# Optimization experiments

Measured on AMD Instinct MI355X. Metric: run time of the kernel, lower is better.

## Reference

```python
import jax, jax.numpy as jnp
import numpy as np

B, P, R_BAR, WIDTH, ADD_WIDTH, KERNEL_WIDTH = 4096, 1024, 64, 1024, 64, 16
NEG_SLOPE = 0.1

def leaky(x):
    return jnp.where(x > 0, x, NEG_SLOPE * x)

def setup_inputs() -> dict:
    key = jax.random.key(0)
    ks = jax.random.split(key, 16)
    s = lambda fan_in: 1.0 / np.sqrt(fan_in)
    return {
        "x": jax.random.normal(ks[0], (B, P), jnp.float32),
        # PCA layer 1: Linear(p -> r_bar), stored [in, out]
        "W_pca": jax.random.normal(ks[1], (P, R_BAR), jnp.float32) * s(P),
        "b_pca": jnp.zeros((R_BAR,), jnp.float32),
        # relu_stack: Linear(r_bar -> width), Linear(width -> width)
        "W1": jax.random.normal(ks[2], (R_BAR, WIDTH), jnp.float32) * s(R_BAR),
        "b1": jnp.zeros((WIDTH,), jnp.float32),
        "W2": jax.random.normal(ks[3], (WIDTH, WIDTH), jnp.float32) * s(WIDTH),
        "b2": jnp.zeros((WIDTH,), jnp.float32),
        # AdditiveLayer 1: r_bar tiny Linears (kernel_width -> add_width), batched [r, in, out]
        "add1_W": jax.random.normal(ks[4], (R_BAR, KERNEL_WIDTH, ADD_WIDTH), jnp.float32) * s(KERNEL_WIDTH),
        "add1_b": jnp.zeros((R_BAR, ADD_WIDTH), jnp.float32),
        "add1_bias": jnp.zeros((1,), jnp.float32),
        # AdditiveLayer 2: r_bar Linears (add_width -> add_width)
        "add2_W": jax.random.normal(ks[5], (R_BAR, ADD_WIDTH, ADD_WIDTH), jnp.float32) * s(ADD_WIDTH),
        "add2_b": jnp.zeros((R_BAR, ADD_WIDTH), jnp.float32),
        "add2_bias": jnp.zeros((1,), jnp.float32),
        # PCA layer 2: Linear(r_bar*add_width -> r_bar)
        "W_pca2": jax.random.normal(ks[6], (R_BAR * ADD_WIDTH, R_BAR), jnp.float32) * s(R_BAR * ADD_WIDTH),
        "b_pca2": jnp.zeros((R_BAR,), jnp.float32),
        # last layer: Linear(r_bar -> 1)
        "W_last": jax.random.normal(ks[7], (R_BAR, 1), jnp.float32) * s(R_BAR),
        "b_last": jnp.zeros((1,), jnp.float32),
    }

def reference(x, W_pca, b_pca, W1, b1, W2, b2,
              add1_W, add1_b, add1_bias,
              add2_W, add2_b, add2_bias,
              W_pca2, b_pca2, W_last, b_last):
    # PcaLayer 1 (cov/trace bookkeeping does not affect the output)
    t = x @ W_pca + b_pca                                   # [B, r_bar]
    # relu_stack (nn_depth = 2)
    h = leaky(t @ W1 + b1)                                   # [B, width]
    h = leaky(h @ W2 + b2)                                   # [B, width]
    # AdditiveLayer 1: modulo-gather kernel_width cols per slot, batched tiny GEMMs
    idx1 = jnp.arange(R_BAR * KERNEL_WIDTH) % h.shape[1]
    g1 = h[:, idx1].reshape(-1, R_BAR, KERNEL_WIDTH)         # [B, r, kw]
    a = jnp.einsum('brk,rko->bro', g1, add1_W) + add1_b      # [B, r, add_w]
    a = leaky(a.reshape(a.shape[0], -1) + add1_bias)         # [B, r*add_w]
    # AdditiveLayer 2: slices are contiguous (mod is identity) -> plain reshape
    g2 = a.reshape(-1, R_BAR, ADD_WIDTH)
    a2 = jnp.einsum('bri,rio->bro', g2, add2_W) + add2_b
    a2 = leaky(a2.reshape(a2.shape[0], -1) + add2_bias)      # [B, r*add_w]
    # PcaLayer 2 + last layer
    t2 = a2 @ W_pca2 + b_pca2                                # [B, r_bar]
    out = (t2 @ W_last + b_last).reshape(-1, 1)              # [B, 1]
    return out
```

## Files before the change

### kernel.cpp

```cpp
#include <hip/hip_runtime.h>

#define NEG_SLOPE 0.1f

__device__ __forceinline__ float leaky(float v) { return v > 0.0f ? v : NEG_SLOPE * v; }

typedef _Float16 h4_t __attribute__((ext_vector_type(4)));
typedef _Float16 h8_t __attribute__((ext_vector_type(8)));
typedef float f32x4 __attribute__((ext_vector_type(4)));

__device__ __forceinline__ unsigned lds_off(const void* p) {
    return (unsigned)(unsigned long long)p;
}

__device__ __forceinline__ void lgkm0() {
    asm volatile("s_waitcnt lgkmcnt(0)" ::: "memory");
    __builtin_amdgcn_sched_barrier(0);
}

__device__ __forceinline__ h4_t tr16(unsigned addr) {
    h4_t d;
    asm volatile("ds_read_b64_tr_b16 %0, %1" : "=v"(d) : "v"(addr) : "memory");
    return d;
}

__global__ __launch_bounds__(256) void prep_weights(const float* __restrict__ W2,
                                                    const float* __restrict__ W1,
                                                    const float* __restrict__ a1W,
                                                    const float* __restrict__ a2W,
                                                    const float* __restrict__ Wp2,
                                                    _Float16* __restrict__ W2T,
                                                    _Float16* __restrict__ W1T,
                                                    _Float16* __restrict__ wpack)
{
    __shared__ float tile[32][33];
    const int b   = blockIdx.x;
    const int tid = threadIdx.x;

    if (b < 1024) {
        const int n0 = (b & 31) * 32, k0 = (b >> 5) * 32;
        const int r = tid >> 3, c4 = (tid & 7) * 4;
        float4 v = *reinterpret_cast<const float4*>(&W2[(size_t)(k0 + r) * 1024 + n0 + c4]);
        tile[r][c4 + 0] = v.x; tile[r][c4 + 1] = v.y;
        tile[r][c4 + 2] = v.z; tile[r][c4 + 3] = v.w;
        __syncthreads();
        h4_t o;
        o[0] = (_Float16)tile[c4 + 0][r]; o[1] = (_Float16)tile[c4 + 1][r];
        o[2] = (_Float16)tile[c4 + 2][r]; o[3] = (_Float16)tile[c4 + 3][r];
        *reinterpret_cast<h4_t*>(&W2T[(size_t)(n0 + r) * 1024 + k0 + c4]) = o;
    } else if (b < 1088) {
        const int b2 = b - 1024;
        const int n0 = (b2 & 31) * 32, k0 = (b2 >> 5) * 32;
        const int r = tid >> 3, c4 = (tid & 7) * 4;
        float4 v = *reinterpret_cast<const float4*>(&W1[(size_t)(k0 + r) * 1024 + n0 + c4]);
        tile[r][c4 + 0] = v.x; tile[r][c4 + 1] = v.y;
        tile[r][c4 + 2] = v.z; tile[r][c4 + 3] = v.w;
        __syncthreads();
        h4_t o;
        o[0] = (_Float16)tile[c4 + 0][r]; o[1] = (_Float16)tile[c4 + 1][r];
        o[2] = (_Float16)tile[c4 + 2][r]; o[3] = (_Float16)tile[c4 + 3][r];
        *reinterpret_cast<h4_t*>(&W1T[(size_t)(n0 + r) * 64 + k0 + c4]) = o;
    } else {
        const int idx = (b - 1088) * 256 + tid;
        if (idx < 589824) {
            const int r = idx / 9216, qq = idx % 9216;
            float v;
            if (qq < 1024) {
                int nt = qq >> 8, rem = qq & 255, l = rem >> 2, j = rem & 3;
                int n = nt * 16 + (l & 15), k = (l >> 4) * 4 + j;
                v = a1W[(size_t)r * 1024 + k * 64 + n];
            } else if (qq < 5120) {
                int p = qq - 1024, kt = p >> 11, u = p & 2047, nt = u >> 9, s = u & 511,
                    l = s >> 3, j = s & 7;
                int n = nt * 16 + (l & 15), k = kt * 32 + (l >> 4) * 8 + j;
                v = a2W[(size_t)r * 4096 + k * 64 + n];
            } else {
                int p = qq - 5120, kt = p >> 11, u = p & 2047, nt = u >> 9, s = u & 511,
                    l = s >> 3, j = s & 7;
                int n = nt * 16 + (l & 15), k = kt * 32 + (l >> 4) * 8 + j;
                v = Wp2[((size_t)r * 64 + k) * 64 + n];
            }
            wpack[idx] = (_Float16)v;
        }
    }
}

__global__ __launch_bounds__(256) void gemm_n64_splitk(const float* __restrict__ A,
                                                       const float* __restrict__ B,
                                                       float* __restrict__ P)
{
    __shared__ alignas(16) float As[32][33];
    __shared__ alignas(16) float Bs[32][64];
    const int tid   = threadIdx.x;
    const int row0  = blockIdx.x * 32;
    const int kbase = blockIdx.y * 128;
    const int r0    = (tid >> 4) * 2;
    const int c0    = (tid & 15) * 4;
    const int am    = tid >> 3;
    const int ak    = (tid & 7) * 4;
    float acc[2][4] = {};

#pragma unroll
    for (int kc = 0; kc < 128; kc += 32) {
        const int k0 = kbase + kc;
        float4 va = *reinterpret_cast<const float4*>(&A[(size_t)(row0 + am) * 1024 + k0 + ak]);
        As[ak + 0][am] = va.x; As[ak + 1][am] = va.y;
        As[ak + 2][am] = va.z; As[ak + 3][am] = va.w;
#pragma unroll
        for (int p = 0; p < 2; ++p) {
            int idx = tid + p * 256;
            int kk  = idx >> 4;
            int nq  = (idx & 15) * 4;
            *reinterpret_cast<float4*>(&Bs[kk][nq]) =
                *reinterpret_cast<const float4*>(&B[(size_t)(k0 + kk) * 64 + nq]);
        }
        __syncthreads();
#pragma unroll
        for (int k = 0; k < 32; ++k) {
            float a0 = As[k][r0], a1 = As[k][r0 + 1];
            float4 bv = *reinterpret_cast<const float4*>(&Bs[k][c0]);
            acc[0][0] = fmaf(a0, bv.x, acc[0][0]); acc[0][1] = fmaf(a0, bv.y, acc[0][1]);
            acc[0][2] = fmaf(a0, bv.z, acc[0][2]); acc[0][3] = fmaf(a0, bv.w, acc[0][3]);
            acc[1][0] = fmaf(a1, bv.x, acc[1][0]); acc[1][1] = fmaf(a1, bv.y, acc[1][1]);
            acc[1][2] = fmaf(a1, bv.z, acc[1][2]); acc[1][3] = fmaf(a1, bv.w, acc[1][3]);
        }
        __syncthreads();
    }
#pragma unroll
    for (int i = 0; i < 2; ++i) {
        float4 o; o.x = acc[i][0]; o.y = acc[i][1]; o.z = acc[i][2]; o.w = acc[i][3];
        *reinterpret_cast<float4*>(
            &P[((size_t)blockIdx.y * 4096 + row0 + r0 + i) * 64 + c0]) = o;
    }
}

__global__ __launch_bounds__(256) void combine_t16(const float* __restrict__ P,
                                                   const float* __restrict__ bias,
                                                   _Float16* __restrict__ t16)
{
    const int idx = blockIdx.x * 256 + threadIdx.x;
    float s = bias[idx & 63];
#pragma unroll
    for (int c = 0; c < 8; ++c)
        s += P[(size_t)c * 262144 + idx];
    t16[idx] = (_Float16)s;
}

__global__ __launch_bounds__(256) void gemm_k64_mfma(const _Float16* __restrict__ A,
                                                     const _Float16* __restrict__ BT,
                                                     const float* __restrict__ bias,
                                                     _Float16* __restrict__ C)
{
    __shared__ alignas(16) _Float16 As[128 * 64];
    __shared__ alignas(16) _Float16 Bs[128 * 64];
    const int tid = threadIdx.x;
    const int l   = tid & 63;
    const int w   = tid >> 6;
    const int wm  = w >> 1;
    const int wn  = w & 1;
    const int bm0 = blockIdx.y * 128;
    const int bn0 = blockIdx.x * 128;
    const int fr  = l & 15;
    const int fg  = l >> 4;
    const int srow  = l >> 3;
    const int sslot = l & 7;

#pragma unroll
    for (int i = 0; i < 4; ++i) {
        const int r0   = w * 32 + i * 8;
        const int rowA = r0 + srow;
        const int slot = sslot ^ (rowA & 7);
        __builtin_amdgcn_global_load_lds(
            (const __attribute__((address_space(1))) void*)&A[(size_t)(bm0 + rowA) * 64 + slot * 8],
            (__attribute__((address_space(3))) void*)&As[r0 * 64], 16, 0, 0);
        __builtin_amdgcn_global_load_lds(
            (const __attribute__((address_space(1))) void*)&BT[(size_t)(bn0 + rowA) * 64 + slot * 8],
            (__attribute__((address_space(3))) void*)&Bs[r0 * 64], 16, 0, 0);
    }
    __syncthreads();

    f32x4 acc[4][4] = {};
#pragma unroll
    for (int ks = 0; ks < 2; ++ks) {
        h8_t af[4], bf[4];
#pragma unroll
        for (int mt = 0; mt < 4; ++mt) {
            int row = wm * 64 + mt * 16 + fr;
            int sg  = ks * 4 + fg;
            af[mt] = *reinterpret_cast<const h8_t*>(&As[row * 64 + ((sg ^ (row & 7)) << 3)]);
        }
#pragma unroll
        for (int nt = 0; nt < 4; ++nt) {
            int row = wn * 64 + nt * 16 + fr;
            int sg  = ks * 4 + fg;
            bf[nt] = *reinterpret_cast<const h8_t*>(&Bs[row * 64 + ((sg ^ (row & 7)) << 3)]);
        }
#pragma unroll
        for (int mt = 0; mt < 4; ++mt)
#pragma unroll
            for (int nt = 0; nt < 4; ++nt)
                acc[mt][nt] = __builtin_amdgcn_mfma_f32_16x16x32_f16(af[mt], bf[nt],
                                                                     acc[mt][nt], 0, 0, 0);
    }

#pragma unroll
    for (int nt = 0; nt < 4; ++nt) {
        const int col = bn0 + wn * 64 + nt * 16 + fr;
        const float bv = bias[col];
#pragma unroll
        for (int mt = 0; mt < 4; ++mt)
#pragma unroll
            for (int rg = 0; rg < 4; ++rg) {
                const int row = bm0 + wm * 64 + mt * 16 + fg * 4 + rg;
                float v = acc[mt][nt][rg] + bv;
                C[(size_t)row * 1024 + col] = (_Float16)fmaxf(v, NEG_SLOPE * v);
            }
    }
}

__global__ __launch_bounds__(256) void gemm_mfma_f16(const _Float16* __restrict__ A,
                                                     const _Float16* __restrict__ BT,
                                                     const float* __restrict__ bias,
                                                     _Float16* __restrict__ h2t)
{
    __shared__ alignas(16) _Float16 As[128 * 32];
    __shared__ alignas(16) _Float16 Bs[128 * 32];
    const int tid = threadIdx.x;
    const int l   = tid & 63;
    const int w   = tid >> 6;
    const int wm  = w >> 1;
    const int wn  = w & 1;
    const int bm0 = blockIdx.y * 128;
    const int bn0 = blockIdx.x * 128;
    const int fr  = l & 15;
    const int fg  = l >> 4;
    const int srow  = l >> 2;
    const int sslot = l & 3;

    f32x4 acc[4][4] = {};

    for (int k0 = 0; k0 < 1024; k0 += 32) {
#pragma unroll
        for (int i = 0; i < 2; ++i) {
            const int r0   = (w * 2 + i) * 16;
            const int rowA = r0 + srow;
            const int slot = sslot ^ (rowA & 3);
            __builtin_amdgcn_global_load_lds(
                (const __attribute__((address_space(1))) void*)&A[(size_t)(bm0 + rowA) * 1024 + k0 + slot * 8],
                (__attribute__((address_space(3))) void*)&As[r0 * 32], 16, 0, 0);
            __builtin_amdgcn_global_load_lds(
                (const __attribute__((address_space(1))) void*)&BT[(size_t)(bn0 + rowA) * 1024 + k0 + slot * 8],
                (__attribute__((address_space(3))) void*)&Bs[r0 * 32], 16, 0, 0);
        }
        __syncthreads();

        h8_t af[4], bf[4];
#pragma unroll
        for (int mt = 0; mt < 4; ++mt) {
            int row = wm * 64 + mt * 16 + fr;
            af[mt] = *reinterpret_cast<const h8_t*>(&As[row * 32 + ((fg ^ (row & 3)) << 3)]);
        }
#pragma unroll
        for (int nt = 0; nt < 4; ++nt) {
            int row = wn * 64 + nt * 16 + fr;
            bf[nt] = *reinterpret_cast<const h8_t*>(&Bs[row * 32 + ((fg ^ (row & 3)) << 3)]);
        }
#pragma unroll
        for (int mt = 0; mt < 4; ++mt)
#pragma unroll
            for (int nt = 0; nt < 4; ++nt)
                acc[mt][nt] = __builtin_amdgcn_mfma_f32_16x16x32_f16(af[mt], bf[nt],
                                                                     acc[mt][nt], 0, 0, 0);
        __syncthreads();
    }

    const int rblk0 = (bm0 >> 4) + wm * 4;
    const int cblk0 = (bn0 >> 4) + wn * 4;
#pragma unroll
    for (int nt = 0; nt < 4; ++nt) {
        const int col = bn0 + wn * 64 + nt * 16 + fr;
        const float bv = bias[col];
#pragma unroll
        for (int mt = 0; mt < 4; ++mt) {
            h4_t pk;
#pragma unroll
            for (int r = 0; r < 4; ++r) {
                float v = acc[mt][nt][r] + bv;
                pk[r] = (_Float16)fmaxf(v, NEG_SLOPE * v);
            }
            *reinterpret_cast<h4_t*>(
                &h2t[(((size_t)(cblk0 + nt) * 256 + rblk0 + mt) * 16 + fr) * 16 + fg * 4]) = pk;
        }
    }
}

#define RCH 4

__global__ __launch_bounds__(256) void fused_tail4(const _Float16* __restrict__ h2t,
                                                   const _Float16* __restrict__ wpack,
                                                   const float* __restrict__ a1b,
                                                   const float* __restrict__ a1bias,
                                                   const float* __restrict__ a2b,
                                                   const float* __restrict__ a2bias,
                                                   float* __restrict__ partials)
{
    __shared__ alignas(16) _Float16 stage[2][10240];
    __shared__ alignas(16) _Float16 act[4][1024];

    const int tid = threadIdx.x;
    const int l = tid & 63, w = tid >> 6;
    const int c = l & 15, q = l >> 4;
    const int row0  = blockIdx.x * 64;
    const int rbase = blockIdx.y * RCH;
    const float b1s = a1bias[0], b2s = a2bias[0];

    const unsigned trl   = l * 8;
    const unsigned abase = lds_off(&act[w][0]);

    float b1v[RCH][4], b2v[RCH][4];
#pragma unroll
    for (int rl = 0; rl < RCH; ++rl)
#pragma unroll
        for (int nt = 0; nt < 4; ++nt) {
            b1v[rl][nt] = a1b[(rbase + rl) * 64 + nt * 16 + c] + b1s;
            b2v[rl][nt] = a2b[(rbase + rl) * 64 + nt * 16 + c] + b2s;
        }

    auto STAGE = [&](int rl, int b) {
        const int r = rbase + rl;
        const _Float16* hsrc = h2t + ((size_t)r * 256 + blockIdx.x * 4) * 256;
        const _Float16* wsrc = wpack + (size_t)r * 9216;
#pragma unroll
        for (int i = 0; i < 5; ++i) {
            const int ch = w * 5 + i;
            const _Float16* src = (ch < 2) ? (hsrc + ch * 512) : (wsrc + (ch - 2) * 512);
            __builtin_amdgcn_global_load_lds(
                (const __attribute__((address_space(1))) void*)(src + l * 8),
                (__attribute__((address_space(3))) void*)&stage[b][ch * 512], 16, 0, 0);
        }
    };

    STAGE(0, 0);
    __syncthreads();

    f32x4 accT[4] = {};
    int cur = 0;

#pragma unroll
    for (int rl = 0; rl < RCH; ++rl) {
        if (rl + 1 < RCH) STAGE(rl + 1, cur ^ 1);

        const _Float16* sp = &stage[cur][0];
        const unsigned sbytes = lds_off(sp);

        h4_t ha = tr16(sbytes + w * 512 + trl);
        lgkm0();
        f32x4 pa[4];
#pragma unroll
        for (int nt = 0; nt < 4; ++nt) {
            h4_t bf = *reinterpret_cast<const h4_t*>(&sp[1024 + nt * 256 + l * 4]);
            pa[nt] = __builtin_amdgcn_mfma_f32_16x16x16f16(ha, bf, (f32x4){0.f,0.f,0.f,0.f}, 0, 0, 0);
        }
#pragma unroll
        for (int nt = 0; nt < 4; ++nt) {
            h4_t pk;
#pragma unroll
            for (int rg = 0; rg < 4; ++rg) {
                float v = pa[nt][rg] + b1v[rl][nt];
                pk[rg] = (_Float16)fmaxf(v, NEG_SLOPE * v);
            }
            const int kk = nt * 16 + c;
            const int hh = (kk >> 2) & 1;
            const int kp = (kk & 3) | ((kk >> 3) << 2);
            *reinterpret_cast<h4_t*>(&act[w][hh * 512 + kp * 16 + q * 4]) = pk;
        }
        lgkm0();

        h8_t afB[2];
#pragma unroll
        for (int kt = 0; kt < 2; ++kt) {
            h4_t lo = tr16(abase + kt * 512 + trl);
            h4_t hi = tr16(abase + 1024 + kt * 512 + trl);
            afB[kt] = __builtin_shufflevector(lo, hi, 0, 1, 2, 3, 4, 5, 6, 7);
        }
        lgkm0();
        f32x4 pb[4] = {};
#pragma unroll
        for (int kt = 0; kt < 2; ++kt)
#pragma unroll
            for (int nt = 0; nt < 4; ++nt) {
                h8_t bf = *reinterpret_cast<const h8_t*>(&sp[2048 + kt * 2048 + nt * 512 + l * 8]);
                pb[nt] = __builtin_amdgcn_mfma_f32_16x16x32_f16(afB[kt], bf, pb[nt], 0, 0, 0);
            }
#pragma unroll
        for (int nt = 0; nt < 4; ++nt) {
            h4_t pk;
#pragma unroll
            for (int rg = 0; rg < 4; ++rg) {
                float v = pb[nt][rg] + b2v[rl][nt];
                pk[rg] = (_Float16)fmaxf(v, NEG_SLOPE * v);
            }
            const int kk = nt * 16 + c;
            const int hh = (kk >> 2) & 1;
            const int kp = (kk & 3) | ((kk >> 3) << 2);
            *reinterpret_cast<h4_t*>(&act[w][hh * 512 + kp * 16 + q * 4]) = pk;
        }
        lgkm0();

        h8_t afC[2];
#pragma unroll
        for (int kt = 0; kt < 2; ++kt) {
            h4_t lo = tr16(abase + kt * 512 + trl);
            h4_t hi = tr16(abase + 1024 + kt * 512 + trl);
            afC[kt] = __builtin_shufflevector(lo, hi, 0, 1, 2, 3, 4, 5, 6, 7);
        }
        lgkm0();
#pragma unroll
        for (int kt = 0; kt < 2; ++kt)
#pragma unroll
            for (int nt = 0; nt < 4; ++nt) {
                h8_t bf = *reinterpret_cast<const h8_t*>(&sp[6144 + kt * 2048 + nt * 512 + l * 8]);
                accT[nt] = __builtin_amdgcn_mfma_f32_16x16x32_f16(afC[kt], bf, accT[nt], 0, 0, 0);
            }

        __syncthreads();
        cur ^= 1;
    }

#pragma unroll
    for (int nt = 0; nt < 4; ++nt)
#pragma unroll
        for (int rg = 0; rg < 4; ++rg)
            partials[((size_t)blockIdx.y * 4096 + row0 + w * 16 + q * 4 + rg) * 64 + nt * 16 + c] =
                accT[nt][rg];
}

__global__ __launch_bounds__(256) void reduce_out(const float* __restrict__ partials,
                                                  const float* __restrict__ bp2,
                                                  const float* __restrict__ Wl,
                                                  const float* __restrict__ bl,
                                                  float* __restrict__ out)
{
    const int tid = threadIdx.x;
    const int row = blockIdx.x * 4 + (tid >> 6);
    const int col = tid & 63;
    float s = bp2[col];
#pragma unroll
    for (int c = 0; c < 16; ++c)
        s += partials[(size_t)c * 262144 + (size_t)row * 64 + col];
    s *= Wl[col];
    s += __shfl_xor(s, 1);
    s += __shfl_xor(s, 2);
    s += __shfl_xor(s, 4);
    s += __shfl_xor(s, 8);
    s += __shfl_xor(s, 16);
    s += __shfl_xor(s, 32);
    if (col == 0) out[row] = s + bl[0];
}

extern "C" void kernel_launch(void* const* d_in, const int* in_sizes, int n_in,
                              void* d_out, int out_size, void* d_ws, size_t ws_size,
                              hipStream_t stream)
{
    const float* x      = (const float*)d_in[0];
    const float* Wpca   = (const float*)d_in[1];
    const float* bpca   = (const float*)d_in[2];
    const float* W1     = (const float*)d_in[3];
    const float* b1     = (const float*)d_in[4];
    const float* W2     = (const float*)d_in[5];
    const float* b2     = (const float*)d_in[6];
    const float* a1W    = (const float*)d_in[7];
    const float* a1b    = (const float*)d_in[8];
    const float* a1bias = (const float*)d_in[9];
    const float* a2W    = (const float*)d_in[10];
    const float* a2b    = (const float*)d_in[11];
    const float* a2bias = (const float*)d_in[12];
    const float* Wp2    = (const float*)d_in[13];
    const float* bp2    = (const float*)d_in[14];
    const float* Wl     = (const float*)d_in[15];
    const float* bl     = (const float*)d_in[16];
    float* out = (float*)d_out;

    char* wsb = (char*)d_ws;
    _Float16* t16      = (_Float16*)(wsb);
    _Float16* h1h      = (_Float16*)(wsb + (1ull  << 20));
    _Float16* h2t      = (_Float16*)(wsb + (9ull  << 20));
    _Float16* W2T      = (_Float16*)(wsb + (17ull << 20));
    _Float16* wpack    = (_Float16*)(wsb + (19ull << 20));
    _Float16* W1T      = (_Float16*)(wsb + (21ull << 20));
    float*    partials = (float*)   (wsb + (22ull << 20));
    float*    tpart    = (float*)   (wsb + (9ull  << 20));

    prep_weights<<<dim3(3392), 256, 0, stream>>>(W2, W1, a1W, a2W, Wp2, W2T, W1T, wpack);
    gemm_n64_splitk<<<dim3(128, 8), 256, 0, stream>>>(x, Wpca, tpart);
    combine_t16<<<dim3(1024), 256, 0, stream>>>(tpart, bpca, t16);
    gemm_k64_mfma<<<dim3(8, 32), 256, 0, stream>>>(t16, W1T, b1, h1h);
    gemm_mfma_f16<<<dim3(8, 32), 256, 0, stream>>>(h1h, W2T, b2, h2t);
    fused_tail4<<<dim3(64, 16), 256, 0, stream>>>(h2t, wpack, a1b, a1bias,
                                                  a2b, a2bias, partials);
    reduce_out<<<dim3(1024), 256, 0, stream>>>(partials, bp2, Wl, bl, out);
}
```

Baseline: 73.58 us.

## Retile W2 GEMM to 64x128 with BK=64 and double rows per tail block

The 1024x1024 GEMM now uses 64x128 output tiles with a 64-deep K step and an 8-way XOR swizzle. This doubles the grid to 512 blocks, which fills the CUs better and halves the number of K iterations and barriers. The fused additive tail kernel now handles 128 batch rows per block instead of 64, so each staged weight tile is reused across two row groups. That halves the weight traffic into LDS, at the cost of more registers and LDS per block and half as many tail blocks.

New measurement: 65.10 us. 1.13x faster.

```diff
diff --git a/kernel.cpp b/kernel.cpp
--- a/kernel.cpp
+++ b/kernel.cpp
@@ -217,70 +217,81 @@
     }
 }
 
-__global__ __launch_bounds__(256) void gemm_mfma_f16(const _Float16* __restrict__ A,
-                                                     const _Float16* __restrict__ BT,
-                                                     const float* __restrict__ bias,
-                                                     _Float16* __restrict__ h2t)
-{
-    __shared__ alignas(16) _Float16 As[128 * 32];
-    __shared__ alignas(16) _Float16 Bs[128 * 32];
+__global__ __launch_bounds__(256) void gemm_mfma_f16_v2(const _Float16* __restrict__ A,
+                                                        const _Float16* __restrict__ BT,
+                                                        const float* __restrict__ bias,
+                                                        _Float16* __restrict__ h2t)
+{
+    __shared__ alignas(16) _Float16 As[64 * 64];
+    __shared__ alignas(16) _Float16 Bs[128 * 64];
     const int tid = threadIdx.x;
     const int l   = tid & 63;
     const int w   = tid >> 6;
     const int wm  = w >> 1;
     const int wn  = w & 1;
-    const int bm0 = blockIdx.y * 128;
+    const int bm0 = blockIdx.y * 64;
     const int bn0 = blockIdx.x * 128;
     const int fr  = l & 15;
     const int fg  = l >> 4;
-    const int srow  = l >> 2;
-    const int sslot = l & 3;
-
-    f32x4 acc[4][4] = {};
-
-    for (int k0 = 0; k0 < 1024; k0 += 32) {
+    const int srow  = l >> 3;
+    const int sslot = l & 7;
+
+    f32x4 acc[2][4] = {};
+
+    for (int k0 = 0; k0 < 1024; k0 += 64) {
 #pragma unroll
         for (int i = 0; i < 2; ++i) {
-            const int r0   = (w * 2 + i) * 16;
+            const int r0   = w * 16 + i * 8;
             const int rowA = r0 + srow;
-            const int slot = sslot ^ (rowA & 3);
+            const int slot = sslot ^ (rowA & 7);
             __builtin_amdgcn_global_load_lds(
                 (const __attribute__((address_space(1))) void*)&A[(size_t)(bm0 + rowA) * 1024 + k0 + slot * 8],
-                (__attribute__((address_space(3))) void*)&As[r0 * 32], 16, 0, 0);
+                (__attribute__((address_space(3))) void*)&As[r0 * 64], 16, 0, 0);
+        }
+#pragma unroll
+        for (int i = 0; i < 4; ++i) {
+            const int r0   = w * 32 + i * 8;
+            const int rowB = r0 + srow;
+            const int slot = sslot ^ (rowB & 7);
             __builtin_amdgcn_global_load_lds(
-                (const __attribute__((address_space(1))) void*)&BT[(size_t)(bn0 + rowA) * 1024 + k0 + slot * 8],
-                (__attribute__((address_space(3))) void*)&Bs[r0 * 32], 16, 0, 0);
-        }
-        __syncthreads();
-
-        h8_t af[4], bf[4];
-#pragma unroll
-        for (int mt = 0; mt < 4; ++mt) {
-            int row = wm * 64 + mt * 16 + fr;
-            af[mt] = *reinterpret_cast<const h8_t*>(&As[row * 32 + ((fg ^ (row & 3)) << 3)]);
-        }
-#pragma unroll
-        for (int nt = 0; nt < 4; ++nt) {
-            int row = wn * 64 + nt * 16 + fr;
-            bf[nt] = *reinterpret_cast<const h8_t*>(&Bs[row * 32 + ((fg ^ (row & 3)) << 3)]);
-        }
-#pragma unroll
-        for (int mt = 0; mt < 4; ++mt)
-#pragma unroll
-            for (int nt = 0; nt < 4; ++nt)
-                acc[mt][nt] = __builtin_amdgcn_mfma_f32_16x16x32_f16(af[mt], bf[nt],
-                                                                     acc[mt][nt], 0, 0, 0);
-        __syncthreads();
-    }
-
-    const int rblk0 = (bm0 >> 4) + wm * 4;
+                (const __attribute__((address_space(1))) void*)&BT[(size_t)(bn0 + rowB) * 1024 + k0 + slot * 8],
+                (__attribute__((address_space(3))) void*)&Bs[r0 * 64], 16, 0, 0);
+        }
+        __syncthreads();
+
+#pragma unroll
+        for (int ks = 0; ks < 2; ++ks) {
+            h8_t af[2], bf[4];
+#pragma unroll
+            for (int mt = 0; mt < 2; ++mt) {
+                int row = wm * 32 + mt * 16 + fr;
+                int sg  = ks * 4 + fg;
+                af[mt] = *reinterpret_cast<const h8_t*>(&As[row * 64 + ((sg ^ (row & 7)) << 3)]);
+            }
+#pragma unroll
+            for (int nt = 0; nt < 4; ++nt) {
+                int row = wn * 64 + nt * 16 + fr;
+                int sg  = ks * 4 + fg;
+                bf[nt] = *reinterpret_cast<const h8_t*>(&Bs[row * 64 + ((sg ^ (row & 7)) << 3)]);
+            }
+#pragma unroll
+            for (int mt = 0; mt < 2; ++mt)
+#pragma unroll
+                for (int nt = 0; nt < 4; ++nt)
+                    acc[mt][nt] = __builtin_amdgcn_mfma_f32_16x16x32_f16(af[mt], bf[nt],
+                                                                         acc[mt][nt], 0, 0, 0);
+        }
+        __syncthreads();
+    }
+
+    const int rblk0 = (bm0 >> 4) + wm * 2;
     const int cblk0 = (bn0 >> 4) + wn * 4;
 #pragma unroll
     for (int nt = 0; nt < 4; ++nt) {
         const int col = bn0 + wn * 64 + nt * 16 + fr;
         const float bv = bias[col];
 #pragma unroll
-        for (int mt = 0; mt < 4; ++mt) {
+        for (int mt = 0; mt < 2; ++mt) {
             h4_t pk;
 #pragma unroll
             for (int r = 0; r < 4; ++r) {
@@ -295,7 +306,7 @@
 
 #define RCH 4
 
-__global__ __launch_bounds__(256) void fused_tail4(const _Float16* __restrict__ h2t,
+__global__ __launch_bounds__(256) void fused_tail5(const _Float16* __restrict__ h2t,
                                                    const _Float16* __restrict__ wpack,
                                                    const float* __restrict__ a1b,
                                                    const float* __restrict__ a1bias,
@@ -303,13 +314,13 @@
                                                    const float* __restrict__ a2bias,
                                                    float* __restrict__ partials)
 {
-    __shared__ alignas(16) _Float16 stage[2][10240];
-    __shared__ alignas(16) _Float16 act[4][1024];
+    __shared__ alignas(16) _Float16 stage[2][11264];
+    __shared__ alignas(16) _Float16 act[4][2048];
 
     const int tid = threadIdx.x;
     const int l = tid & 63, w = tid >> 6;
     const int c = l & 15, q = l >> 4;
-    const int row0  = blockIdx.x * 64;
+    const int row0  = blockIdx.x * 128;
     const int rbase = blockIdx.y * RCH;
     const float b1s = a1bias[0], b2s = a2bias[0];
 
@@ -327,22 +338,24 @@
 
     auto STAGE = [&](int rl, int b) {
         const int r = rbase + rl;
-        const _Float16* hsrc = h2t + ((size_t)r * 256 + blockIdx.x * 4) * 256;
+        const _Float16* hsrc = h2t + ((size_t)r * 256 + blockIdx.x * 8) * 256;
         const _Float16* wsrc = wpack + (size_t)r * 9216;
 #pragma unroll
-        for (int i = 0; i < 5; ++i) {
-            const int ch = w * 5 + i;
-            const _Float16* src = (ch < 2) ? (hsrc + ch * 512) : (wsrc + (ch - 2) * 512);
-            __builtin_amdgcn_global_load_lds(
-                (const __attribute__((address_space(1))) void*)(src + l * 8),
-                (__attribute__((address_space(3))) void*)&stage[b][ch * 512], 16, 0, 0);
+        for (int i = 0; i < 6; ++i) {
+            const int ch = i * 4 + w;
+            if (ch < 22) {
+                const _Float16* src = (ch < 4) ? (hsrc + ch * 512) : (wsrc + (ch - 4) * 512);
+                __builtin_amdgcn_global_load_lds(
+                    (const __attribute__((address_space(1))) void*)(src + l * 8),
+                    (__attribute__((address_space(3))) void*)&stage[b][ch * 512], 16, 0, 0);
+            }
         }
     };
 
     STAGE(0, 0);
     __syncthreads();
 
-    f32x4 accT[4] = {};
+    f32x4 accT[2][4] = {};
     int cur = 0;
 
 #pragma unroll
@@ -352,74 +365,86 @@
         const _Float16* sp = &stage[cur][0];
         const unsigned sbytes = lds_off(sp);
 
-        h4_t ha = tr16(sbytes + w * 512 + trl);
+        h4_t ha0 = tr16(sbytes + (unsigned)(w) * 512 + trl);
+        h4_t ha1 = tr16(sbytes + (unsigned)(w + 4) * 512 + trl);
         lgkm0();
-        f32x4 pa[4];
+        f32x4 pa[2][4];
 #pragma unroll
         for (int nt = 0; nt < 4; ++nt) {
-            h4_t bf = *reinterpret_cast<const h4_t*>(&sp[1024 + nt * 256 + l * 4]);
-            pa[nt] = __builtin_amdgcn_mfma_f32_16x16x16f16(ha, bf, (f32x4){0.f,0.f,0.f,0.f}, 0, 0, 0);
-        }
-#pragma unroll
-        for (int nt = 0; nt < 4; ++nt) {
-            h4_t pk;
-#pragma unroll
-            for (int rg = 0; rg < 4; ++rg) {
-                float v = pa[nt][rg] + b1v[rl][nt];
-                pk[rg] = (_Float16)fmaxf(v, NEG_SLOPE * v);
-            }
-            const int kk = nt * 16 + c;
-            const int hh = (kk >> 2) & 1;
-            const int kp = (kk & 3) | ((kk >> 3) << 2);
-            *reinterpret_cast<h4_t*>(&act[w][hh * 512 + kp * 16 + q * 4]) = pk;
-        }
+            h4_t bf = *reinterpret_cast<const h4_t*>(&sp[2048 + nt * 256 + l * 4]);
+            pa[0][nt] = __builtin_amdgcn_mfma_f32_16x16x16f16(ha0, bf, (f32x4){0.f,0.f,0.f,0.f}, 0, 0, 0);
+            pa[1][nt] = __builtin_amdgcn_mfma_f32_16x16x16f16(ha1, bf, (f32x4){0.f,0.f,0.f,0.f}, 0, 0, 0);
+        }
+#pragma unroll
+        for (int j = 0; j < 2; ++j)
+#pragma unroll
+            for (int nt = 0; nt < 4; ++nt) {
+                h4_t pk;
+#pragma unroll
+                for (int rg = 0; rg < 4; ++rg) {
+                    float v = pa[j][nt][rg] + b1v[rl][nt];
+                    pk[rg] = (_Float16)fmaxf(v, NEG_SLOPE * v);
+                }
+                const int kk = nt * 16 + c;
+                const int hh = (kk >> 2) & 1;
+                const int kp = (kk & 3) | ((kk >> 3) << 2);
+                *reinterpret_cast<h4_t*>(&act[w][j * 1024 + hh * 512 + kp * 16 + q * 4]) = pk;
+            }
         lgkm0();
 
-        h8_t afB[2];
-#pragma unroll
-        for (int kt = 0; kt < 2; ++kt) {
-            h4_t lo = tr16(abase + kt * 512 + trl);
-            h4_t hi = tr16(abase + 1024 + kt * 512 + trl);
-            afB[kt] = __builtin_shufflevector(lo, hi, 0, 1, 2, 3, 4, 5, 6, 7);
-        }
+        h8_t afB[2][2];
+#pragma unroll
+        for (int j = 0; j < 2; ++j)
+#pragma unroll
+            for (int kt = 0; kt < 2; ++kt) {
+                h4_t lo = tr16(abase + (unsigned)(j * 2048 + kt * 512) + trl);
+                h4_t hi = tr16(abase + (unsigned)(j * 2048 + 1024 + kt * 512) + trl);
+                afB[j][kt] = __builtin_shufflevector(lo, hi, 0, 1, 2, 3, 4, 5, 6, 7);
+            }
         lgkm0();
-        f32x4 pb[4] = {};
+        f32x4 pb[2][4] = {};
 #pragma unroll
         for (int kt = 0; kt < 2; ++kt)
 #pragma unroll
             for (int nt = 0; nt < 4; ++nt) {
-                h8_t bf = *reinterpret_cast<const h8_t*>(&sp[2048 + kt * 2048 + nt * 512 + l * 8]);
-                pb[nt] = __builtin_amdgcn_mfma_f32_16x16x32_f16(afB[kt], bf, pb[nt], 0, 0, 0);
-            }
-#pragma unroll
-        for (int nt = 0; nt < 4; ++nt) {
-            h4_t pk;
-#pragma unroll
-            for (int rg = 0; rg < 4; ++rg) {
-                float v = pb[nt][rg] + b2v[rl][nt];
-                pk[rg] = (_Float16)fmaxf(v, NEG_SLOPE * v);
-            }
-            const int kk = nt * 16 + c;
-            const int hh = (kk >> 2) & 1;
-            const int kp = (kk & 3) | ((kk >> 3) << 2);
-            *reinterpret_cast<h4_t*>(&act[w][hh * 512 + kp * 16 + q * 4]) = pk;
-        }
+                h8_t bf = *reinterpret_cast<const h8_t*>(&sp[3072 + kt * 2048 + nt * 512 + l * 8]);
+                pb[0][nt] = __builtin_amdgcn_mfma_f32_16x16x32_f16(afB[0][kt], bf, pb[0][nt], 0, 0, 0);
+                pb[1][nt] = __builtin_amdgcn_mfma_f32_16x16x32_f16(afB[1][kt], bf, pb[1][nt], 0, 0, 0);
+            }
+#pragma unroll
+        for (int j = 0; j < 2; ++j)
+#pragma unroll
+            for (int nt = 0; nt < 4; ++nt) {
+                h4_t pk;
+#pragma unroll
+                for (int rg = 0; rg < 4; ++rg) {
+                    float v = pb[j][nt][rg] + b2v[rl][nt];
+                    pk[rg] = (_Float16)fmaxf(v, NEG_SLOPE * v);
+                }
+                const int kk = nt * 16 + c;
+                const int hh = (kk >> 2) & 1;
+                const int kp = (kk & 3) | ((kk >> 3) << 2);
+                *reinterpret_cast<h4_t*>(&act[w][j * 1024 + hh * 512 + kp * 16 + q * 4]) = pk;
+            }
         lgkm0();
 
-        h8_t afC[2];
-#pragma unroll
-        for (int kt = 0; kt < 2; ++kt) {
-            h4_t lo = tr16(abase + kt * 512 + trl);
-            h4_t hi = tr16(abase + 1024 + kt * 512 + trl);
-            afC[kt] = __builtin_shufflevector(lo, hi, 0, 1, 2, 3, 4, 5, 6, 7);
-        }
+        h8_t afC[2][2];
+#pragma unroll
+        for (int j = 0; j < 2; ++j)
+#pragma unroll
+            for (int kt = 0; kt < 2; ++kt) {
+                h4_t lo = tr16(abase + (unsigned)(j * 2048 + kt * 512) + trl);
+                h4_t hi = tr16(abase + (unsigned)(j * 2048 + 1024 + kt * 512) + trl);
+                afC[j][kt] = __builtin_shufflevector(lo, hi, 0, 1, 2, 3, 4, 5, 6, 7);
+            }
         lgkm0();
 #pragma unroll
         for (int kt = 0; kt < 2; ++kt)
 #pragma unroll
             for (int nt = 0; nt < 4; ++nt) {
-                h8_t bf = *reinterpret_cast<const h8_t*>(&sp[6144 + kt * 2048 + nt * 512 + l * 8]);
-                accT[nt] = __builtin_amdgcn_mfma_f32_16x16x32_f16(afC[kt], bf, accT[nt], 0, 0, 0);
+                h8_t bf = *reinterpret_cast<const h8_t*>(&sp[7168 + kt * 2048 + nt * 512 + l * 8]);
+                accT[0][nt] = __builtin_amdgcn_mfma_f32_16x16x32_f16(afC[0][kt], bf, accT[0][nt], 0, 0, 0);
+                accT[1][nt] = __builtin_amdgcn_mfma_f32_16x16x32_f16(afC[1][kt], bf, accT[1][nt], 0, 0, 0);
             }
 
         __syncthreads();
@@ -427,11 +452,13 @@
     }
 
 #pragma unroll
-    for (int nt = 0; nt < 4; ++nt)
-#pragma unroll
-        for (int rg = 0; rg < 4; ++rg)
-            partials[((size_t)blockIdx.y * 4096 + row0 + w * 16 + q * 4 + rg) * 64 + nt * 16 + c] =
-                accT[nt][rg];
+    for (int j = 0; j < 2; ++j)
+#pragma unroll
+        for (int nt = 0; nt < 4; ++nt)
+#pragma unroll
+            for (int rg = 0; rg < 4; ++rg)
+                partials[((size_t)blockIdx.y * 4096 + row0 + (w + 4 * j) * 16 + q * 4 + rg) * 64
+                         + nt * 16 + c] = accT[j][nt][rg];
 }
 
 __global__ __launch_bounds__(256) void reduce_out(const float* __restrict__ partials,
@@ -494,8 +521,8 @@
     gemm_n64_splitk<<<dim3(128, 8), 256, 0, stream>>>(x, Wpca, tpart);
     combine_t16<<<dim3(1024), 256, 0, stream>>>(tpart, bpca, t16);
     gemm_k64_mfma<<<dim3(8, 32), 256, 0, stream>>>(t16, W1T, b1, h1h);
-    gemm_mfma_f16<<<dim3(8, 32), 256, 0, stream>>>(h1h, W2T, b2, h2t);
-    fused_tail4<<<dim3(64, 16), 256, 0, stream>>>(h2t, wpack, a1b, a1bias,
+    gemm_mfma_f16_v2<<<dim3(8, 64), 256, 0, stream>>>(h1h, W2T, b2, h2t);
+    fused_tail5<<<dim3(32, 16), 256, 0, stream>>>(h2t, wpack, a1b, a1bias,
                                                   a2b, a2bias, partials);
     reduce_out<<<dim3(1024), 256, 0, stream>>>(partials, bp2, Wl, bl, out);
 }
```
